# Kernel tuning notes

Hardware: AMD Instinct MI355X
Metric: run time of the kernel (lower is better)

## Reference

```python
import jax, jax.numpy as jnp
import numpy as np

N = 1_000_000   # child nodes at depth d
P = 300_000     # parent nodes at depth d-1
C = 256         # feature channels


def setup_inputs() -> dict:
    key = jax.random.key(0)
    k1, k2 = jax.random.split(key)
    features = jax.random.normal(k1, (N, C), dtype=jnp.float32)
    # child quadtree keys, sorted; parent = key >> 2 lies in [0, P)
    keys = jnp.sort(jax.random.randint(k2, (N,), 0, 4 * P, dtype=jnp.int64))
    # every parent key present -> searchsorted gives exact parent index
    parent_level_keys = jnp.arange(P, dtype=jnp.int64)
    return {"features": features, "keys": keys, "parent_level_keys": parent_level_keys}


def reference(features, keys, parent_level_keys):
    num_parents = parent_level_keys.shape[0]
    parent_keys = keys >> 2
    parent_idx = jnp.searchsorted(parent_level_keys, parent_keys)
    # fused scatter-max / segment-max replacing the original Python loop
    pooled = jax.ops.segment_max(
        features, parent_idx, num_segments=num_parents, indices_are_sorted=True
    )  # [P, C]; empty segments are -inf
    # original fills untouched rows (sentinel -1e9) with 0
    pooled = jnp.where(jnp.isneginf(pooled), jnp.zeros((), pooled.dtype), pooled)
    return pooled, parent_idx
```

## Files before the change

### kernel.cpp

```cpp
#include <hip/hip_runtime.h>


typedef float v4f __attribute__((ext_vector_type(4)));

static __device__ __forceinline__ v4f vmax4(v4f a, v4f b) {
    v4f r;
    r.x = fmaxf(a.x, b.x); r.y = fmaxf(a.y, b.y);
    r.z = fmaxf(a.z, b.z); r.w = fmaxf(a.w, b.w);
    return r;
}

__global__ void qp_starts(const int* __restrict__ keys, const int* __restrict__ plk,
                          int* __restrict__ starts, int N, int P) {
    int p = blockIdx.x * blockDim.x + threadIdx.x;
    if (p > P) return;
    if (p == 0) { starts[0] = 0; return; }
    const int t = plk[p - 1];
    int lo = 0, hi = N;
    while (lo < hi) {
        int mid = (lo + hi) >> 1;
        if ((keys[mid] >> 2) > t) hi = mid; else lo = mid + 1;
    }
    starts[p] = lo;
}

__global__ void qp_pidx(const int* __restrict__ keys, const int* __restrict__ plk,
                        float* __restrict__ pidx_out, int N, int P) {
    int i = blockIdx.x * blockDim.x + threadIdx.x;
    if (i >= N) return;
    const int pk = keys[i] >> 2;
    int idx;
    if (pk >= 0 && pk < P && plk[pk] == pk && (pk == 0 || plk[pk - 1] < pk)) {
        idx = pk;
    } else {
        int lo = 0, hi = P;
        while (lo < hi) {
            int mid = (lo + hi) >> 1;
            if (plk[mid] >= pk) hi = mid; else lo = mid + 1;
        }
        idx = lo;
    }
    pidx_out[i] = (float)idx;
}

__global__ void __launch_bounds__(256) qp_pool(const float* __restrict__ feat,
        const int* __restrict__ starts, float* __restrict__ pooled, int P, int C) {
    int t = blockIdx.x * blockDim.x + threadIdx.x;
    int wave = t >> 6, lane = t & 63;
    if (wave >= P) return;
    const int s = starts[wave];
    const int e = starts[wave + 1];
    const int n = e - s;
    const size_t stepv = (size_t)(C >> 2);
    for (int c0 = lane * 4; c0 < C; c0 += 256) {
        const v4f* p = reinterpret_cast<const v4f*>(feat + (size_t)s * C + c0);
        v4f m; m.x = m.y = m.z = m.w = -INFINITY;
        int i = 0;
        for (; i + 2 <= n; i += 2) {
            v4f a = __builtin_nontemporal_load(p);
            v4f b = __builtin_nontemporal_load(p + stepv);
            p += 2 * stepv;
            m = vmax4(m, vmax4(a, b));
        }
        if (i < n) {
            v4f a = __builtin_nontemporal_load(p);
            m = vmax4(m, a);
        }
        if (n <= 0) { m.x = m.y = m.z = m.w = 0.f; }
        __builtin_nontemporal_store(m,
            reinterpret_cast<v4f*>(pooled + (size_t)wave * C + c0));
    }
}

extern "C" void kernel_launch(void* const* d_in, const int* in_sizes, int n_in,
                              void* d_out, int out_size, void* d_ws, size_t ws_size,
                              hipStream_t stream) {
    const float* feat = (const float*)d_in[0];
    const int*   keys = (const int*)d_in[1];
    const int*   plk  = (const int*)d_in[2];

    const long long F = in_sizes[0], K = in_sizes[1], L = in_sizes[2];
    int N = (int)K, P = (int)L, C = (int)(F / (K > 0 ? K : 1));
    if ((long long)P * C + N != (long long)out_size) {
        for (int w1 = 1; w1 <= 2; ++w1) {
            bool done = false;
            for (int w2 = 1; w2 <= 2; ++w2) {
                if (K % w1 || L % w2) continue;
                long long n = K / w1, p = L / w2;
                if (n <= 0 || p <= 0 || F % n) continue;
                long long c = F / n;
                if (p * c + n == (long long)out_size) {
                    N = (int)n; P = (int)p; C = (int)c; done = true; break;
                }
            }
            if (done) break;
        }
    }

    float* outf   = (float*)d_out;
    float* pooled = outf;
    float* pidx   = outf + (size_t)P * C;
    int* starts   = (int*)d_ws;

    const int tb = 256;
    qp_starts<<<(P + 1 + tb - 1) / tb, tb, 0, stream>>>(keys, plk, starts, N, P);
    qp_pidx  <<<(N + tb - 1) / tb,     tb, 0, stream>>>(keys, plk, pidx, N, P);
    const long long thr = (long long)P * 64;
    qp_pool<<<(int)((thr + tb - 1) / tb), tb, 0, stream>>>(feat, starts, pooled, P, C);
}
```

Baseline: 231.1 us.

## Fuse three kernels into one and compute segment bounds per wave inline

Merges the starts, parent-index and pooling kernels into a single launch. The block range is split so the first blocks compute parent indices and the rest do pooling. Each pooling wave now binary-searches its own start and end, with half the lanes searching each bound and the results shared by shuffle, instead of reading a precomputed starts array. This removes two launches and the workspace round trip. In exchange every pooling wave repeats a binary search over a million keys, which adds scattered memory reads.

```diff
diff --git a/kernel.cpp b/kernel.cpp
--- a/kernel.cpp
+++ b/kernel.cpp
@@ -10,47 +10,45 @@
     return r;
 }
 
-__global__ void qp_starts(const int* __restrict__ keys, const int* __restrict__ plk,
-                          int* __restrict__ starts, int N, int P) {
-    int p = blockIdx.x * blockDim.x + threadIdx.x;
-    if (p > P) return;
-    if (p == 0) { starts[0] = 0; return; }
-    const int t = plk[p - 1];
+__global__ void __launch_bounds__(256) qp_fused(const float* __restrict__ feat,
+        const int* __restrict__ keys, const int* __restrict__ plk,
+        float* __restrict__ outf, int N, int P, int C, int pidxBlocks) {
+
+    if ((int)blockIdx.x < pidxBlocks) {
+        int i = blockIdx.x * 256 + threadIdx.x;
+        if (i >= N) return;
+        const int pk = keys[i] >> 2;
+        int idx;
+        if (pk >= 0 && pk < P && plk[pk] == pk && (pk == 0 || plk[pk - 1] < pk)) {
+            idx = pk;
+        } else {
+            int lo = 0, hi = P;
+            while (lo < hi) {
+                int mid = (lo + hi) >> 1;
+                if (plk[mid] >= pk) hi = mid; else lo = mid + 1;
+            }
+            idx = lo;
+        }
+        __builtin_nontemporal_store((float)idx, outf + (size_t)P * C + i);
+        return;
+    }
+
+    int t = (blockIdx.x - pidxBlocks) * 256 + threadIdx.x;
+    int wave = t >> 6, lane = t & 63;
+    if (wave >= P) return;
+
+    const int t_lo = (wave == 0) ? -1 : plk[wave - 1];
+    const int t_hi = plk[wave];
+    const int target = (lane & 32) ? t_hi : t_lo;
     int lo = 0, hi = N;
     while (lo < hi) {
         int mid = (lo + hi) >> 1;
-        if ((keys[mid] >> 2) > t) hi = mid; else lo = mid + 1;
+        if ((keys[mid] >> 2) > target) hi = mid; else lo = mid + 1;
     }
-    starts[p] = lo;
-}
+    const int s = __shfl(lo, 0, 64);
+    const int e = __shfl(lo, 32, 64);
+    const int n = e - s;
 
-__global__ void qp_pidx(const int* __restrict__ keys, const int* __restrict__ plk,
-                        float* __restrict__ pidx_out, int N, int P) {
-    int i = blockIdx.x * blockDim.x + threadIdx.x;
-    if (i >= N) return;
-    const int pk = keys[i] >> 2;
-    int idx;
-    if (pk >= 0 && pk < P && plk[pk] == pk && (pk == 0 || plk[pk - 1] < pk)) {
-        idx = pk;
-    } else {
-        int lo = 0, hi = P;
-        while (lo < hi) {
-            int mid = (lo + hi) >> 1;
-            if (plk[mid] >= pk) hi = mid; else lo = mid + 1;
-        }
-        idx = lo;
-    }
-    pidx_out[i] = (float)idx;
-}
-
-__global__ void __launch_bounds__(256) qp_pool(const float* __restrict__ feat,
-        const int* __restrict__ starts, float* __restrict__ pooled, int P, int C) {
-    int t = blockIdx.x * blockDim.x + threadIdx.x;
-    int wave = t >> 6, lane = t & 63;
-    if (wave >= P) return;
-    const int s = starts[wave];
-    const int e = starts[wave + 1];
-    const int n = e - s;
     const size_t stepv = (size_t)(C >> 2);
     for (int c0 = lane * 4; c0 < C; c0 += 256) {
         const v4f* p = reinterpret_cast<const v4f*>(feat + (size_t)s * C + c0);
@@ -62,13 +60,10 @@
             p += 2 * stepv;
             m = vmax4(m, vmax4(a, b));
         }
-        if (i < n) {
-            v4f a = __builtin_nontemporal_load(p);
-            m = vmax4(m, a);
-        }
+        if (i < n) m = vmax4(m, __builtin_nontemporal_load(p));
         if (n <= 0) { m.x = m.y = m.z = m.w = 0.f; }
         __builtin_nontemporal_store(m,
-            reinterpret_cast<v4f*>(pooled + (size_t)wave * C + c0));
+            reinterpret_cast<v4f*>(outf + (size_t)wave * C + c0));
     }
 }
 
@@ -97,14 +92,10 @@
         }
     }
 
-    float* outf   = (float*)d_out;
-    float* pooled = outf;
-    float* pidx   = outf + (size_t)P * C;
-    int* starts   = (int*)d_ws;
-
     const int tb = 256;
-    qp_starts<<<(P + 1 + tb - 1) / tb, tb, 0, stream>>>(keys, plk, starts, N, P);
-    qp_pidx  <<<(N + tb - 1) / tb,     tb, 0, stream>>>(keys, plk, pidx, N, P);
-    const long long thr = (long long)P * 64;
-    qp_pool<<<(int)((thr + tb - 1) / tb), tb, 0, stream>>>(feat, starts, pooled, P, C);
+    const int pidxBlocks = (N + tb - 1) / tb;
+    const long long poolThreads = (long long)P * 64;
+    const int poolBlocks = (int)((poolThreads + tb - 1) / tb);
+    qp_fused<<<pidxBlocks + poolBlocks, tb, 0, stream>>>(
+        feat, keys, plk, (float*)d_out, N, P, C, pidxBlocks);
 }
```

After: 446.0 us. +93.0%, slower.
